# Performance work log

Measured on AMD Instinct MI355X. Metric: run time of the kernel, lower is better.

Reference implementation:

```python
import jax, jax.numpy as jnp
import numpy as np

SEARCH_RANGE = 4  # matches init_kwargs


def setup_inputs() -> dict:
    key = jax.random.key(0)
    k1, k2 = jax.random.split(key)
    shape = (8, 256, 64, 128)  # [B, C, H, W]
    feature1 = jax.random.normal(k1, shape, dtype=jnp.float32)
    feature2 = jax.random.normal(k2, shape, dtype=jnp.float32)
    return {"feature1": feature1, "feature2": feature2}


def reference(feature1, feature2):
    R = SEARCH_RANGE
    b, c, h, w = feature1.shape
    # zero-pad feature2 spatially by R on each side
    f2p = jnp.pad(feature2, ((0, 0), (0, 0), (R, R), (R, R)))
    D = 2 * R + 1
    # shift offsets in the same order as the original nested loop (idx outer, jdx inner)
    offsets = jnp.stack(
        jnp.meshgrid(jnp.arange(D), jnp.arange(D), indexing="ij"), axis=-1
    ).reshape(-1, 2)  # [81, 2]

    def corr_one(ij):
        win = jax.lax.dynamic_slice(f2p, (0, 0, ij[0], ij[1]), (b, c, h, w))
        return jnp.sum(feature1 * win, axis=1)  # [B, H, W]

    dots = jax.vmap(corr_one)(offsets)  # [81, B, H, W]
    return jnp.transpose(dots, (1, 0, 2, 3))  # [B, 81, H, W]
```

## Files before the change

### kernel.cpp

```cpp
#include <hip/hip_runtime.h>
#include <cstdint>

typedef __attribute__((ext_vector_type(8))) short short8;
typedef __attribute__((ext_vector_type(4))) float floatx4;
typedef __attribute__((ext_vector_type(2))) unsigned int uintx2;
typedef __attribute__((ext_vector_type(4))) unsigned int uintx4;

__device__ __forceinline__ uint32_t pack2(float a, float b) {
    uint32_t ua = __builtin_bit_cast(uint32_t, a);
    uint32_t ub = __builtin_bit_cast(uint32_t, b);
    ua = (ua + 0x7FFFu + ((ua >> 16) & 1u)) >> 16;
    ub = (ub + 0x7FFFu + ((ub >> 16) & 1u)) >> 16;
    return ua | (ub << 16);
}

#define T2P_WORDS ((size_t)8 * 64 * 144 * 128)
#define WS_NEED   (T2P_WORDS * 4 + 4096)

__global__ __launch_bounds__(256)
void transpose_f2(const float* __restrict__ f2, uint32_t* __restrict__ t2p) {
    __shared__ float t[64][33];
    const int tid = threadIdx.x;
    const int bid = blockIdx.x;
    const int b = bid & 7, h = (bid >> 3) & 63, wt = bid >> 9;
    const int w0 = wt * 32;
    const float* f2b = f2 + (size_t)b * 256 * 8192 + (size_t)h * 128 + w0;
    uint32_t* t2row = t2p + ((size_t)(b * 64 + h) * 144 + (w0 + 4)) * 128;

    const int rw = tid & 31, rc8 = tid >> 5;
    const int kpL = tid & 31, wg = tid >> 5;

    for (int cc = 0; cc < 4; ++cc) {
        if (cc) __syncthreads();
#pragma unroll
        for (int i = 0; i < 8; ++i)
            t[rc8 * 8 + i][rw] = f2b[(size_t)(cc * 64 + rc8 * 8 + i) * 8192 + rw];
        __syncthreads();
#pragma unroll
        for (int j = 0; j < 4; ++j) {
            int w = wg * 4 + j;
            t2row[(size_t)w * 128 + cc * 32 + kpL] = pack2(t[2 * kpL][w], t[2 * kpL + 1][w]);
        }
    }
    if (wt == 0) {
        uint32_t* p = t2p + ((size_t)(b * 64 + h) * 144) * 128;
        for (int idx = tid; idx < 512; idx += 256) p[idx] = 0;
    }
    if (wt == 3) {
        uint32_t* p = t2p + ((size_t)(b * 64 + h) * 144 + 132) * 128;
        for (int idx = tid; idx < 1536; idx += 256) p[idx] = 0;
    }
    if (bid == 0) {
        uint32_t* z = t2p + T2P_WORDS;
        for (int idx = tid; idx < 1024; idx += 256) z[idx] = 0;
    }
}

#define AS1 __attribute__((address_space(1)))
#define AS3 __attribute__((address_space(3)))

__device__ __forceinline__ void gld_lds16(const uint32_t* src, uint32_t* dst) {
    __builtin_amdgcn_global_load_lds((const AS1 void*)src, (AS3 void*)dst, 16, 0, 0);
}

__global__ __launch_bounds__(512, 3)
void corr2(const float* __restrict__ f1, const uint32_t* __restrict__ t2p,
           const uint32_t* __restrict__ wsZ, float* __restrict__ out) {
    __shared__ uint32_t ldsB[2 * 8192];

    const int tid  = threadIdx.x;
    const int lane = tid & 63;
    const int wh   = tid >> 6;
    const int n15  = lane & 15;
    const int q    = lane >> 4;

    const int bid = blockIdx.x;
    const int b  = bid & 7;
    const int ht = (bid >> 3) & 7;
    const int wt = bid >> 6;
    const int h0 = 8 * ht, w0 = 16 * wt;
    const int h  = h0 + wh;
    const int p  = (ht + wt) & 7;

    const float* f1b = f1 + (size_t)b * 256 * 8192;

    const uint32_t* bbase[4];
    int bstep[4], bdst[4];
#pragma unroll
    for (int ki = 0; ki < 4; ++ki) {
        int k = 4 * wh + ki, r = k >> 1, gh = h0 - 4 + r;
        int c = (k & 1) * 16 + (lane >> 2);
        int gd = (lane & 3) ^ ((c >> 1) & 3);
        bool ok = (unsigned)gh < 64u;
        bbase[ki] = ok ? t2p + ((size_t)(b * 64 + gh) * 144 + (w0 + c)) * 128 + gd * 4
                       : wsZ + lane * 4;
        bstep[ki] = ok ? 16 : 0;
        bdst[ki]  = k * 256;
    }

    const float* aBase = f1b + (size_t)h * 128 + w0 + n15;

    floatx4 acc[9][2];
#pragma unroll
    for (int di = 0; di < 9; ++di)
#pragma unroll
        for (int t = 0; t < 2; ++t)
            acc[di][t] = (floatx4){0.f, 0.f, 0.f, 0.f};

    const int rdB = n15 * 16 + ((q ^ ((n15 >> 1) & 3)) << 2);

    auto stageB = [&](int bufsel, int cc) {
        uint32_t* dst = ldsB + bufsel * 8192;
#pragma unroll
        for (int ki = 0; ki < 4; ++ki)
            gld_lds16(bbase[ki] + (size_t)cc * bstep[ki], &dst[bdst[ki]]);
    };
    auto loadA = [&](float* r, int cc) {
        const float* ap = aBase + (size_t)(32 * cc + 8 * q) * 8192;
#pragma unroll
        for (int j = 0; j < 8; ++j) r[j] = ap[(size_t)j * 8192];
    };
    auto packA = [&](const float* r) -> short8 {
        uintx4 av = {pack2(r[0], r[1]), pack2(r[2], r[3]),
                     pack2(r[4], r[5]), pack2(r[6], r[7])};
        return __builtin_bit_cast(short8, av);
    };
    auto mfma9 = [&](int bufsel, short8 a0) {
        const uint32_t* bufB = ldsB + bufsel * 8192;
#pragma unroll
        for (int di = 0; di < 9; ++di) {
            const uint32_t* p0 = bufB + (wh + di) * 512 + rdB;
            uintx4 v0 = *(const uintx4*)p0;
            uintx4 v1 = *(const uintx4*)(p0 + 128);
            short8 b0 = __builtin_bit_cast(short8, v0);
            short8 b1 = __builtin_bit_cast(short8, v1);
            acc[di][0] = __builtin_amdgcn_mfma_f32_16x16x32_bf16(a0, b0, acc[di][0], 0, 0, 0);
            acc[di][1] = __builtin_amdgcn_mfma_f32_16x16x32_bf16(a0, b1, acc[di][1], 0, 0, 0);
        }
    };

    float rA0[8], rA1[8];

    stageB(0, p);
    __builtin_amdgcn_sched_barrier(0);
    loadA(rA0, p);
    __builtin_amdgcn_sched_barrier(0);
    stageB(1, (p + 1) & 7);
    __builtin_amdgcn_sched_barrier(0);
    loadA(rA1, (p + 1) & 7);
    __builtin_amdgcn_sched_barrier(0);

#define CHUNK(K, VM, RS)                                                      \
    {                                                                         \
        asm volatile("s_waitcnt vmcnt(" #VM ")\n\ts_barrier" ::: "memory");   \
        if ((K) >= 1 && (K) < 7) stageB(((K) + 1) & 1, ((K) + 1 + p) & 7);    \
        __builtin_amdgcn_sched_barrier(0);                                    \
        short8 a0 = packA(RS);                                                \
        if ((K) < 6) loadA(RS, ((K) + 2 + p) & 7);                            \
        __builtin_amdgcn_sched_barrier(0);                                    \
        mfma9((K) & 1, a0);                                                   \
    }

    CHUNK(0, 20, rA0)
    CHUNK(1, 16, rA1)
    CHUNK(2, 8,  rA0)
    CHUNK(3, 8,  rA1)
    CHUNK(4, 8,  rA0)
    CHUNK(5, 8,  rA1)
    CHUNK(6, 8,  rA0)
    CHUNK(7, 0,  rA1)
#undef CHUNK

    const size_t base = ((size_t)b * 81) * 8192 + (size_t)h * 128 + w0;
#pragma unroll
    for (int di = 0; di < 9; ++di) {
#pragma unroll
        for (int t = 0; t < 2; ++t) {
#pragma unroll
            for (int r = 0; r < 4; ++r) {
                int mp = 4 * q + r;
                int dj = t * 8 + n15 - mp;
                if (dj >= 0 && dj <= 8 && (t == 0 || n15 >= 8)) {
                    out[base + (size_t)(di * 9 + dj) * 8192 + mp] = acc[di][t][r];
                }
            }
        }
    }
}

#define CS 18
#define A_WORDS (8 * 16 * CS)
#define B_ROWS  13
#define B_WORDS (B_ROWS * 24 * CS)

__device__ __forceinline__ short8 frag_ld(const uint32_t* p) {
    uintx2 lo = *(const uintx2*)p;
    uintx2 hi = *(const uintx2*)(p + 2);
    uintx4 v = {lo.x, lo.y, hi.x, hi.y};
    return __builtin_bit_cast(short8, v);
}

__global__ __launch_bounds__(512, 4)
void corr_kernel(const float* __restrict__ f1, const float* __restrict__ f2,
                 float* __restrict__ out) {
    __shared__ uint32_t ldsA[2 * A_WORDS];
    __shared__ uint32_t ldsB2[2 * B_WORDS];

    const int tid  = threadIdx.x;
    const int lane = tid & 63;
    const int wh   = tid >> 6;
    const int n15  = lane & 15;
    const int q    = lane >> 4;

    const int bid    = blockIdx.x;
    const int b      = bid & 7;
    const int dihalf = (bid >> 3) & 1;
    const int ht     = (bid >> 4) & 7;
    const int wt     = bid >> 7;

    const int w0 = wt * 16;
    const int h0 = ht * 8;
    const int h  = h0 + wh;

    const int diN    = dihalf ? 4 : 5;
    const int diBase = dihalf * 5;
    const int ghBase = dihalf ? (h0 + 1) : (h0 - 4);

    const float* f1b = f1 + (size_t)b * 256 * 8192;
    const float* f2b = f2 + (size_t)b * 256 * 8192;

    const int aw4 = tid & 3, akp = (tid >> 2) & 15, arow = tid >> 6;
    int aOffG = (2 * akp) * 8192 + (h0 + arow) * 128 + (w0 + 4 * aw4);
    const int aLds = (arow * 16 + 4 * aw4) * CS + akp;

    int bOffG[3]; int bLds[3]; uint32_t bMask[3];
#pragma unroll
    for (int s = 0; s < 3; ++s) {
        int t = tid + 512 * s;
        int w4 = t % 6;
        int r2 = t / 6;
        int kp = r2 & 15, row = r2 >> 4;
        int gh = ghBase + row;
        int gw = w0 - 4 + 4 * w4;
        bool live = (t < 1152);
        bool inb  = live && ((unsigned)gh < 64u) && ((unsigned)gw < 128u);
        bOffG[s] = inb ? ((2 * kp) * 8192 + gh * 128 + gw) : 0;
        bLds[s]  = live ? ((row * 24 + 4 * w4) * CS + kp) : ((12 * 24 + (tid & 7)) * CS);
        bMask[s] = inb ? 0xFFFFFFFFu : 0u;
    }

    floatx4 acc[5][2];
#pragma unroll
    for (int dl = 0; dl < 5; ++dl)
#pragma unroll
        for (int t = 0; t < 2; ++t)
            acc[dl][t] = (floatx4){0.f, 0.f, 0.f, 0.f};

    floatx4 rA[2], rB[3][2];
    uint32_t pkA[4], pkB[12];

    auto issue = [&]() {
        rA[0] = *(const floatx4*)(f1b + aOffG);
        rA[1] = *(const floatx4*)(f1b + aOffG + 8192);
        aOffG += 32 * 8192;
#pragma unroll
        for (int s = 0; s < 3; ++s) {
            rB[s][0] = *(const floatx4*)(f2b + bOffG[s]);
            rB[s][1] = *(const floatx4*)(f2b + bOffG[s] + 8192);
            bOffG[s] += 32 * 8192;
        }
    };
    auto packall = [&]() {
#pragma unroll
        for (int i = 0; i < 4; ++i) pkA[i] = pack2(rA[0][i], rA[1][i]);
#pragma unroll
        for (int s = 0; s < 3; ++s)
#pragma unroll
            for (int i = 0; i < 4; ++i)
                pkB[4 * s + i] = pack2(rB[s][0][i], rB[s][1][i]) & bMask[s];
    };

    issue(); packall();

    for (int ch = 0; ch < 8; ++ch) {
        uint32_t* bufA = ldsA + (ch & 1) * A_WORDS;
        uint32_t* bufB = ldsB2 + (ch & 1) * B_WORDS;
#pragma unroll
        for (int i = 0; i < 4; ++i) bufA[aLds + i * CS] = pkA[i];
#pragma unroll
        for (int s = 0; s < 3; ++s)
#pragma unroll
            for (int i = 0; i < 4; ++i) bufB[bLds[s] + i * CS] = pkB[4 * s + i];
        if (ch < 7) issue();
        __syncthreads();

        const uint32_t* pa = bufA + (wh * 16 + n15) * CS + 4 * q;
        short8 a0 = frag_ld(pa);
        const uint32_t* pb = bufB + (wh * 24 + n15) * CS + 4 * q;
#pragma unroll
        for (int dl = 0; dl < 5; ++dl) {
            if (dl < diN) {
                const uint32_t* pp = pb + dl * (24 * CS);
                short8 b0 = frag_ld(pp);
                short8 b1 = frag_ld(pp + 8 * CS);
                acc[dl][0] = __builtin_amdgcn_mfma_f32_16x16x32_bf16(a0, b0, acc[dl][0], 0, 0, 0);
                acc[dl][1] = __builtin_amdgcn_mfma_f32_16x16x32_bf16(a0, b1, acc[dl][1], 0, 0, 0);
            }
        }
        if (ch < 7) packall();
    }

    const size_t base = ((size_t)b * 81) * 8192 + (size_t)h * 128 + w0;
#pragma unroll
    for (int dl = 0; dl < 5; ++dl) {
        if (dl < diN) {
            const int dio = diBase + dl;
#pragma unroll
            for (int t = 0; t < 2; ++t) {
#pragma unroll
                for (int r = 0; r < 4; ++r) {
                    int mp = 4 * q + r;
                    int dj = t * 8 + n15 - mp;
                    if (dj >= 0 && dj <= 8 && (t == 0 || n15 >= 8)) {
                        out[base + (size_t)(dio * 9 + dj) * 8192 + mp] = acc[dl][t][r];
                    }
                }
            }
        }
    }
}

extern "C" void kernel_launch(void* const* d_in, const int* in_sizes, int n_in,
                              void* d_out, int out_size, void* d_ws, size_t ws_size,
                              hipStream_t stream) {
    const float* f1 = (const float*)d_in[0];
    const float* f2 = (const float*)d_in[1];
    float* out = (float*)d_out;
    if (ws_size >= WS_NEED && d_ws != nullptr) {
        uint32_t* t2p = (uint32_t*)d_ws;
        transpose_f2<<<dim3(2048), dim3(256), 0, stream>>>(f2, t2p);
        corr2<<<dim3(512), dim3(512), 0, stream>>>(f1, t2p, t2p + T2P_WORDS, out);
    } else {
        corr_kernel<<<dim3(1024), dim3(512), 0, stream>>>(f1, f2, out);
    }
}
```

Measured before the change: 184.2 us.

## Split transposed feature2 into per-channel-chunk slabs and drop rotated chunk order

```diff
diff --git a/kernel.cpp b/kernel.cpp
--- a/kernel.cpp
+++ b/kernel.cpp
@@ -14,7 +14,8 @@
     return ua | (ub << 16);
 }
 
-#define T2P_WORDS ((size_t)8 * 64 * 144 * 128)
+#define CC_SLAB  ((size_t)8 * 64 * 2304)
+#define T2P_WORDS (8 * CC_SLAB)
 #define WS_NEED   (T2P_WORDS * 4 + 4096)
 
 __global__ __launch_bounds__(256)
@@ -25,10 +26,10 @@
     const int b = bid & 7, h = (bid >> 3) & 63, wt = bid >> 9;
     const int w0 = wt * 32;
     const float* f2b = f2 + (size_t)b * 256 * 8192 + (size_t)h * 128 + w0;
-    uint32_t* t2row = t2p + ((size_t)(b * 64 + h) * 144 + (w0 + 4)) * 128;
 
     const int rw = tid & 31, rc8 = tid >> 5;
-    const int kpL = tid & 31, wg = tid >> 5;
+    const int tp = tid & 127, rr = tid >> 7;
+    const int m  = tp & 15;
 
     for (int cc = 0; cc < 4; ++cc) {
         if (cc) __syncthreads();
@@ -36,19 +37,27 @@
         for (int i = 0; i < 8; ++i)
             t[rc8 * 8 + i][rw] = f2b[(size_t)(cc * 64 + rc8 * 8 + i) * 8192 + rw];
         __syncthreads();
-#pragma unroll
-        for (int j = 0; j < 4; ++j) {
-            int w = wg * 4 + j;
-            t2row[(size_t)w * 128 + cc * 32 + kpL] = pack2(t[2 * kpL][w], t[2 * kpL + 1][w]);
+        const int cc2 = 2 * cc + rr;
+        uint32_t* dst = t2p + (size_t)cc2 * CC_SLAB
+                        + ((size_t)b * 64 + h) * 2304 + (size_t)(w0 + 4) * 16;
+#pragma unroll
+        for (int i = 0; i < 4; ++i) {
+            int d = i * 128 + tp;
+            int j = d >> 4;
+            dst[d] = pack2(t[rr * 32 + 2 * m][j], t[rr * 32 + 2 * m + 1][j]);
         }
     }
     if (wt == 0) {
-        uint32_t* p = t2p + ((size_t)(b * 64 + h) * 144) * 128;
-        for (int idx = tid; idx < 512; idx += 256) p[idx] = 0;
+        for (int idx = tid; idx < 512; idx += 256) {
+            int cc2 = idx >> 6, o = idx & 63;
+            t2p[(size_t)cc2 * CC_SLAB + ((size_t)b * 64 + h) * 2304 + o] = 0;
+        }
     }
     if (wt == 3) {
-        uint32_t* p = t2p + ((size_t)(b * 64 + h) * 144 + 132) * 128;
-        for (int idx = tid; idx < 1536; idx += 256) p[idx] = 0;
+        for (int idx = tid; idx < 1536; idx += 256) {
+            int cc2 = idx / 192, o = idx % 192;
+            t2p[(size_t)cc2 * CC_SLAB + ((size_t)b * 64 + h) * 2304 + 132 * 16 + o] = 0;
+        }
     }
     if (bid == 0) {
         uint32_t* z = t2p + T2P_WORDS;
@@ -80,21 +89,21 @@
     const int wt = bid >> 6;
     const int h0 = 8 * ht, w0 = 16 * wt;
     const int h  = h0 + wh;
-    const int p  = (ht + wt) & 7;
 
     const float* f1b = f1 + (size_t)b * 256 * 8192;
 
     const uint32_t* bbase[4];
-    int bstep[4], bdst[4];
+    size_t bstep[4];
+    int bdst[4];
 #pragma unroll
     for (int ki = 0; ki < 4; ++ki) {
         int k = 4 * wh + ki, r = k >> 1, gh = h0 - 4 + r;
         int c = (k & 1) * 16 + (lane >> 2);
         int gd = (lane & 3) ^ ((c >> 1) & 3);
         bool ok = (unsigned)gh < 64u;
-        bbase[ki] = ok ? t2p + ((size_t)(b * 64 + gh) * 144 + (w0 + c)) * 128 + gd * 4
+        bbase[ki] = ok ? t2p + ((size_t)b * 64 + gh) * 2304 + (size_t)(w0 + c) * 16 + gd * 4
                        : wsZ + lane * 4;
-        bstep[ki] = ok ? 16 : 0;
+        bstep[ki] = ok ? CC_SLAB : 0;
         bdst[ki]  = k * 256;
     }
 
@@ -141,22 +150,22 @@
 
     float rA0[8], rA1[8];
 
-    stageB(0, p);
+    stageB(0, 0);
     __builtin_amdgcn_sched_barrier(0);
-    loadA(rA0, p);
+    loadA(rA0, 0);
     __builtin_amdgcn_sched_barrier(0);
-    stageB(1, (p + 1) & 7);
+    stageB(1, 1);
     __builtin_amdgcn_sched_barrier(0);
-    loadA(rA1, (p + 1) & 7);
+    loadA(rA1, 1);
     __builtin_amdgcn_sched_barrier(0);
 
 #define CHUNK(K, VM, RS)                                                      \
     {                                                                         \
         asm volatile("s_waitcnt vmcnt(" #VM ")\n\ts_barrier" ::: "memory");   \
-        if ((K) >= 1 && (K) < 7) stageB(((K) + 1) & 1, ((K) + 1 + p) & 7);    \
+        if ((K) >= 1 && (K) < 7) stageB(((K) + 1) & 1, (K) + 1);              \
         __builtin_amdgcn_sched_barrier(0);                                    \
         short8 a0 = packA(RS);                                                \
-        if ((K) < 6) loadA(RS, ((K) + 2 + p) & 7);                            \
+        if ((K) < 6) loadA(RS, (K) + 2);                                      \
         __builtin_amdgcn_sched_barrier(0);                                    \
         mfma9((K) & 1, a0);                                                   \
     }
```

Result: faster. 177.3 us (-3.7%).
